# Optimization experiments

Measured on AMD Instinct MI355X. Metric: run time of the kernel, lower is better.

The kernel has to match this reference:

```python
import jax, jax.numpy as jnp
import numpy as np

EPS = 1e-5
N_HEADS = 8
CLAMP = 100.0


def layernorm(x, g, b):
    m = x.mean(-1, keepdims=True)
    v = x.var(-1, keepdims=True)  # biased var, matches torch LayerNorm
    return (x - m) / jnp.sqrt(v + EPS) * g + b


def depthwise7(x, w, b):
    # x: [B,C,H,W], w: [C,1,7,7] depthwise (groups=C), pad=3
    y = jax.lax.conv_general_dilated(
        x, w, window_strides=(1, 1), padding=[(3, 3), (3, 3)],
        dimension_numbers=('NCHW', 'OIHW', 'NCHW'),
        feature_group_count=x.shape[1])
    return y + b[None, :, None, None]


def setup_inputs() -> dict:
    key = jax.random.key(0)
    ks = jax.random.split(key, 12)
    B, N, C = 8, 4096, 512
    KH = 7
    s = 0.02
    return {
        'x': jax.random.normal(ks[0], (B, N, C), jnp.float32),
        'qkv_w': jax.random.normal(ks[1], (C, 3 * C), jnp.float32) * s,
        'qkv_b': jnp.zeros((3 * C,), jnp.float32),
        'out_w': jax.random.normal(ks[2], (C, C), jnp.float32) * s,
        'out_b': jnp.zeros((C,), jnp.float32),
        'pre_g': jnp.ones((C,), jnp.float32),
        'pre_b': jnp.zeros((C,), jnp.float32),
        'lcm_g': jnp.ones((C,), jnp.float32),
        'lcm_b': jnp.zeros((C,), jnp.float32),
        'ci_w': jax.random.normal(ks[3], (C, 1, KH, KH), jnp.float32) * s,
        'ci_b': jnp.zeros((C,), jnp.float32),
        'bn_g': jnp.ones((C,), jnp.float32),
        'bn_b': jnp.zeros((C,), jnp.float32),
        'co_w': jax.random.normal(ks[4], (C, 1, KH, KH), jnp.float32) * s,
        'co_b': jnp.zeros((C,), jnp.float32),
        'H': 64,
        'W': 64,
    }


def reference(x, qkv_w, qkv_b, out_w, out_b, pre_g, pre_b, lcm_g, lcm_b,
              ci_w, ci_b, bn_g, bn_b, co_w, co_b, H, W):
    B, N, C = x.shape
    hd = C // N_HEADS
    normed = layernorm(x, pre_g, pre_b)
    qkv = normed @ qkv_w + qkv_b                       # [B,N,3C]
    qkv = qkv.reshape(B, N, 3, N_HEADS, hd).transpose(2, 0, 3, 1, 4)
    q = jax.nn.relu(qkv[0])                            # [B,h,N,d]
    k = jax.nn.relu(qkv[1])
    v = qkv[2]
    kv = jnp.einsum('bhnd,bhnv->bhdv', k, v)           # O(N d^2) associativity trick
    normalizer = jnp.maximum(k.sum(2, keepdims=True), CLAMP)  # [B,h,1,d]
    attn = jnp.einsum('bhnd,bhdv->bhnv', q, kv)
    denom = jnp.maximum((q * normalizer).sum(-1, keepdims=True), CLAMP)
    attn = attn / denom
    attn = attn.transpose(0, 2, 1, 3).reshape(B, N, C)
    attn = attn @ out_w + out_b
    # Local Concentration Module on lcm_norm(attn)
    t = layernorm(attn, lcm_g, lcm_b)
    xi = t.transpose(0, 2, 1).reshape(B, C, H, W)
    y = depthwise7(xi, ci_w, ci_b)
    y = jax.nn.gelu(y, approximate=False)
    m = y.mean((0, 2, 3), keepdims=True)               # BatchNorm2d training-mode stats
    var = y.var((0, 2, 3), keepdims=True)
    y = (y - m) / jnp.sqrt(var + EPS) * bn_g[None, :, None, None] + bn_b[None, :, None, None]
    y = depthwise7(y, co_w, co_b)
    lcm_out = y.reshape(B, C, N).transpose(0, 2, 1)
    return x + attn + lcm_out
```

## Files before the change

### kernel.cpp

```cpp
#include <hip/hip_runtime.h>
#include <math.h>

typedef short v8s __attribute__((ext_vector_type(8)));
typedef short v4s __attribute__((ext_vector_type(4)));
typedef float v4f __attribute__((ext_vector_type(4)));

__device__ __forceinline__ float b2f(unsigned short u) {
    return __uint_as_float(((unsigned)u) << 16);
}
__device__ __forceinline__ unsigned short f2b(float f) {
    unsigned u = __float_as_uint(f);
    unsigned r = (u + 0x7FFF + ((u >> 16) & 1)) >> 16;
    return (unsigned short)r;
}

__device__ __forceinline__ void gl_lds16(const unsigned short* g, unsigned short* l) {
    __builtin_amdgcn_global_load_lds(
        (const __attribute__((address_space(1))) void*)g,
        (__attribute__((address_space(3))) void*)l,
        16, 0, 0);
}

__global__ __launch_bounds__(256) void zero_fill(float* __restrict__ p, int n) {
    int i = blockIdx.x * 256 + threadIdx.x;
    if (i < n) p[i] = 0.0f;
}

__global__ __launch_bounds__(256) void ln_apply(const float* __restrict__ x,
                                                const float* __restrict__ g,
                                                const float* __restrict__ bt,
                                                unsigned short* __restrict__ out) {
    size_t row = blockIdx.x;
    const float2* p = (const float2*)(x + row * 512);
    int t = threadIdx.x;
    float2 v = p[t];
    float s = v.x + v.y, s2 = v.x * v.x + v.y * v.y;
    for (int o = 32; o > 0; o >>= 1) {
        s += __shfl_down(s, o);
        s2 += __shfl_down(s2, o);
    }
    __shared__ float rs[4], rq[4];
    int wave = t >> 6, lane = t & 63;
    if (lane == 0) { rs[wave] = s; rq[wave] = s2; }
    __syncthreads();
    float ts = rs[0] + rs[1] + rs[2] + rs[3];
    float tq = rq[0] + rq[1] + rq[2] + rq[3];
    float mean = ts * (1.0f / 512.0f);
    float var = tq * (1.0f / 512.0f) - mean * mean;
    float inv = rsqrtf(var + 1e-5f);
    float2 gg = ((const float2*)g)[t];
    float2 bb = ((const float2*)bt)[t];
    ushort2 o2;
    o2.x = f2b((v.x - mean) * inv * gg.x + bb.x);
    o2.y = f2b((v.y - mean) * inv * gg.y + bb.y);
    *(ushort2*)&out[row * 512 + 2 * t] = o2;
}

__global__ __launch_bounds__(256) void transpose_f2b(const float* __restrict__ in,
                                                     unsigned short* __restrict__ out,
                                                     int R, int C) {
    __shared__ unsigned short tile[32][33];
    int c0 = blockIdx.x * 32, r0 = blockIdx.y * 32;
    int tx = threadIdx.x, ty = threadIdx.y;
    for (int j = 0; j < 32; j += 8)
        tile[ty + j][tx] = f2b(in[(size_t)(r0 + ty + j) * C + c0 + tx]);
    __syncthreads();
    for (int j = 0; j < 32; j += 8)
        out[(size_t)(c0 + ty + j) * R + r0 + tx] = tile[tx][ty + j];
}

template <int NB, bool QKV>
__global__ __launch_bounds__(512, 2) void gemm256(const unsigned short* __restrict__ A,
                                                  const unsigned short* __restrict__ Bt,
                                                  const float* __restrict__ bias,
                                                  unsigned short* __restrict__ o0,
                                                  unsigned short* __restrict__ o1,
                                                  unsigned short* __restrict__ o2) {
    __shared__ __align__(16) unsigned short LB[4][2][8192];
    int t = threadIdx.x;
    int wave = t >> 6, lane = t & 63;
    int wm = wave >> 2, wn = wave & 3;
    int mrow = lane & 15, kq4 = lane >> 4;
    int nwg = gridDim.x;
    int cpx = nwg >> 3;
    int bid = blockIdx.x;
    int swz = (bid & 7) * cpx + (bid >> 3);
    int n0 = (swz % NB) * 256;
    int m0 = (swz / NB) * 256;
    const unsigned short* Ab = A + (size_t)m0 * 512;
    const unsigned short* Bb = Bt + (size_t)n0 * 512;
    int g0 = wave * 128 + lane;
    int g1 = g0 + 64;
    int r0 = g0 >> 2, c0 = ((g0 & 3) ^ ((r0 >> 1) & 3)) * 8;
    int r1 = g1 >> 2, c1 = ((g1 & 3) ^ ((r1 >> 1) & 3)) * 8;
    size_t src0 = (size_t)r0 * 512 + c0;
    size_t src1 = (size_t)r1 * 512 + c1;
    unsigned ldsOff0 = wave * 1024;
    unsigned ldsOff1 = wave * 1024 + 512;
    v4f acc[8][4] = {};
    int swr = ((kq4 ^ ((mrow >> 1) & 3)) * 8);

#define STAGE(kt, slot)                                          \
    do {                                                         \
        const unsigned short* aS = Ab + (size_t)(kt) * 32;       \
        const unsigned short* bS = Bb + (size_t)(kt) * 32;       \
        gl_lds16(aS + src0, &LB[slot][0][ldsOff0]);              \
        gl_lds16(aS + src1, &LB[slot][0][ldsOff1]);              \
        gl_lds16(bS + src0, &LB[slot][1][ldsOff0]);              \
        gl_lds16(bS + src1, &LB[slot][1][ldsOff1]);              \
    } while (0)

    STAGE(0, 0);
    STAGE(1, 1);
    for (int kt = 0; kt < 16; ++kt) {
        if (kt < 15) {
            asm volatile("s_waitcnt vmcnt(4)" ::: "memory");
        } else {
            asm volatile("s_waitcnt vmcnt(0)" ::: "memory");
        }
        __builtin_amdgcn_s_barrier();
        asm volatile("" ::: "memory");
        if (kt + 2 < 16) {
            int slot2 = (kt + 2) & 3;
            STAGE(kt + 2, slot2);
        }
        const unsigned short* as = LB[kt & 3][0];
        const unsigned short* bs = LB[kt & 3][1];
        v8s af[8], bf[4];
#pragma unroll
        for (int i = 0; i < 8; i++)
            af[i] = *(const v8s*)&as[(wm * 128 + i * 16 + mrow) * 32 + swr];
#pragma unroll
        for (int j = 0; j < 4; j++)
            bf[j] = *(const v8s*)&bs[(wn * 64 + j * 16 + mrow) * 32 + swr];
        __builtin_amdgcn_s_setprio(1);
#pragma unroll
        for (int i = 0; i < 8; i++)
#pragma unroll
            for (int j = 0; j < 4; j++)
                acc[i][j] = __builtin_amdgcn_mfma_f32_16x16x32_bf16(af[i], bf[j], acc[i][j], 0, 0, 0);
        __builtin_amdgcn_s_setprio(0);
    }
#undef STAGE
    __syncthreads();
    unsigned short* CT = &LB[0][0][0];
    bool doRelu = QKV && (n0 < 1024);
#pragma unroll
    for (int j = 0; j < 4; j++) {
        int col = wn * 64 + j * 16 + mrow;
        float bv = bias[n0 + col];
        int gr = col >> 3;
        int gb = col & 7;
#pragma unroll
        for (int i = 0; i < 8; i++) {
            int rowb = wm * 128 + i * 16 + kq4 * 4;
#pragma unroll
            for (int r = 0; r < 4; r++) {
                int row = rowb + r;
                float v = acc[i][j][r] + bv;
                if (doRelu) v = fmaxf(v, 0.0f);
                CT[row * 256 + ((gr ^ (row & 7)) << 3) + gb] = f2b(v);
            }
        }
    }
    __syncthreads();
    unsigned short* base;
    if (QKV) {
        int seg = n0 >> 9;
        base = (seg == 0) ? o0 : ((seg == 1) ? o1 : o2);
    } else {
        base = o0;
    }
    int cb = n0 & 511;
#pragma unroll
    for (int p = 0; p < 16; p++) {
        int g = p * 512 + t;
        int row = g >> 5, gl = g & 31;
        int phys = gl ^ (row & 7);
        v8s v = *(const v8s*)&CT[row * 256 + (phys << 3)];
        *(v8s*)&base[(size_t)(m0 + row) * 512 + cb + gl * 8] = v;
    }
}

__global__ __launch_bounds__(256) void kv_part(const unsigned short* __restrict__ kbuf,
                                               const unsigned short* __restrict__ vbuf,
                                               float* __restrict__ kvp,
                                               float* __restrict__ ksp) {
    int bh = blockIdx.x;
    int b = bh >> 3, h = bh & 7;
    int nc = blockIdx.y;
    __shared__ __align__(16) unsigned short kb[64 * 64];
    __shared__ __align__(16) unsigned short vb[64 * 64];
    int t = threadIdx.x;
    int dk0 = (t >> 4) * 4;
    int dv0 = (t & 15) * 4;
    float acc[4][4] = {};
    float ks[4] = {};
    int lr = t >> 2, lc = (t & 3) * 16;
    for (int n0 = nc * 128; n0 < nc * 128 + 128; n0 += 64) {
        __syncthreads();
        size_t base = ((size_t)(b * 4096 + n0 + lr)) * 512 + h * 64;
        *(v8s*)&kb[lr * 64 + lc]     = *(const v8s*)&kbuf[base + lc];
        *(v8s*)&kb[lr * 64 + lc + 8] = *(const v8s*)&kbuf[base + lc + 8];
        *(v8s*)&vb[lr * 64 + lc]     = *(const v8s*)&vbuf[base + lc];
        *(v8s*)&vb[lr * 64 + lc + 8] = *(const v8s*)&vbuf[base + lc + 8];
        __syncthreads();
#pragma unroll 4
        for (int nn = 0; nn < 64; nn++) {
            v4s kr = *(const v4s*)&kb[nn * 64 + dk0];
            v4s vr = *(const v4s*)&vb[nn * 64 + dv0];
            float kf[4], vf[4];
#pragma unroll
            for (int i = 0; i < 4; i++) { kf[i] = b2f((unsigned short)kr[i]); vf[i] = b2f((unsigned short)vr[i]); }
#pragma unroll
            for (int i = 0; i < 4; i++) {
#pragma unroll
                for (int j = 0; j < 4; j++) acc[i][j] += kf[i] * vf[j];
            }
            if ((t & 15) == 0) {
#pragma unroll
                for (int i = 0; i < 4; i++) ks[i] += kf[i];
            }
        }
    }
    float* dst = kvp + ((size_t)(bh * 32 + nc)) * 4096;
#pragma unroll
    for (int i = 0; i < 4; i++)
        *(float4*)&dst[(dk0 + i) * 64 + dv0] = make_float4(acc[i][0], acc[i][1], acc[i][2], acc[i][3]);
    if ((t & 15) == 0) {
        float* kd = ksp + ((size_t)(bh * 32 + nc)) * 64;
#pragma unroll
        for (int i = 0; i < 4; i++) kd[dk0 + i] = ks[i];
    }
}

__global__ __launch_bounds__(256) void kv_reduce(const float* __restrict__ kvp,
                                                 const float* __restrict__ ksp,
                                                 float* __restrict__ kvb,
                                                 float* __restrict__ ksum) {
    int tid = blockIdx.x * 256 + threadIdx.x;
    int bh = tid >> 12, e = tid & 4095;
    float s = 0.0f;
#pragma unroll 8
    for (int c = 0; c < 32; c++) s += kvp[((size_t)(bh * 32 + c)) * 4096 + e];
    kvb[(size_t)bh * 4096 + e] = s;
    if (tid < 4096) {
        int bh2 = tid >> 6, dk = tid & 63;
        float t = 0.0f;
#pragma unroll 8
        for (int c = 0; c < 32; c++) t += ksp[((size_t)(bh2 * 32 + c)) * 64 + dk];
        ksum[tid] = t;
    }
}

__global__ __launch_bounds__(256) void attn_kernel(unsigned short* qa,
                                                   const float* __restrict__ kv,
                                                   const float* __restrict__ ksum) {
    int bh = blockIdx.y;
    int b = bh >> 3, h = bh & 7;
    int nt = blockIdx.x;
    __shared__ float kvs[64 * 64];
    __shared__ float nrm[64];
    int t = threadIdx.x;
    for (int i = t; i < 4096; i += 256) kvs[i] = kv[(size_t)bh * 4096 + i];
    if (t < 64) nrm[t] = fmaxf(ksum[bh * 64 + t], 100.0f);
    __syncthreads();
    int n = nt * 256 + t;
    unsigned short* qp = qa + ((size_t)(b * 4096 + n)) * 512 + h * 64;
    float qf[64];
#pragma unroll
    for (int i = 0; i < 64; i += 8) {
        v8s v = *(const v8s*)&qp[i];
#pragma unroll
        for (int j = 0; j < 8; j++) qf[i + j] = b2f((unsigned short)v[j]);
    }
    float denom = 0.0f;
#pragma unroll
    for (int d = 0; d < 64; d++) denom += qf[d] * nrm[d];
    denom = fmaxf(denom, 100.0f);
    float inv = 1.0f / denom;
#pragma unroll
    for (int dv = 0; dv < 64; dv += 16) {
        float o[16] = {};
        for (int dk = 0; dk < 64; dk++) {
            float q = qf[dk];
#pragma unroll
            for (int i = 0; i < 16; i++) o[i] += q * kvs[dk * 64 + dv + i];
        }
#pragma unroll
        for (int i = 0; i < 16; i++) qp[dv + i] = f2b(o[i] * inv);
    }
}

__global__ __launch_bounds__(256) void ln2_transpose(const unsigned short* __restrict__ in,
                                                     const float* __restrict__ g,
                                                     const float* __restrict__ bt,
                                                     unsigned short* __restrict__ out) {
    int bid = blockIdx.x;
    int b = bid >> 6;
    int n0 = (bid & 63) * 64;
    __shared__ float gs[512], bs[512];
    __shared__ __align__(16) unsigned short tile[512 * 64];
    int t = threadIdx.x;
    for (int i = t; i < 512; i += 256) { gs[i] = g[i]; bs[i] = bt[i]; }
    int nl = t >> 2, sub = t & 3;
    const unsigned short* src = in + ((size_t)(b * 4096 + n0 + nl)) * 512 + sub * 8;
    v8s vv[16];
#pragma unroll
    for (int c16 = 0; c16 < 16; c16++)
        vv[c16] = *(const v8s*)&src[c16 * 32];
    float s = 0.f, s2 = 0.f;
#pragma unroll
    for (int c16 = 0; c16 < 16; c16++)
#pragma unroll
        for (int j = 0; j < 8; j++) {
            float f = b2f((unsigned short)vv[c16][j]);
            s += f; s2 += f * f;
        }
    s += __shfl_xor(s, 1); s2 += __shfl_xor(s2, 1);
    s += __shfl_xor(s, 2); s2 += __shfl_xor(s2, 2);
    float mean = s * (1.f / 512.f);
    float var = s2 * (1.f / 512.f) - mean * mean;
    float inv = rsqrtf(var + 1e-5f);
    __syncthreads();
#pragma unroll
    for (int c16 = 0; c16 < 16; c16++) {
        int cb_ = sub * 8 + c16 * 32;
#pragma unroll
        for (int j = 0; j < 8; j++) {
            int c = cb_ + j;
            float f = b2f((unsigned short)vv[c16][j]);
            float y = (f - mean) * inv * gs[c] + bs[c];
            tile[c * 64 + ((((nl >> 3) ^ (c & 7)) << 3) | (nl & 7))] = f2b(y);
        }
    }
    __syncthreads();
    unsigned short* dst = out + ((size_t)b * 512) * 4096 + n0;
#pragma unroll
    for (int p = 0; p < 16; p++) {
        int chunk = p * 256 + t;
        int c = chunk >> 3, gseg = chunk & 7;
        int phys = gseg ^ (c & 7);
        v8s v = *(const v8s*)&tile[c * 64 + phys * 8];
        *(v8s*)&dst[(size_t)c * 4096 + gseg * 8] = v;
    }
}

__global__ __launch_bounds__(256) void dwconv7_gelu(const unsigned short* __restrict__ in,
                                                    const float* __restrict__ w,
                                                    const float* __restrict__ bias,
                                                    unsigned short* __restrict__ out,
                                                    float* __restrict__ bn_sum,
                                                    float* __restrict__ bn_sumsq) {
    int bc = blockIdx.x;
    int c = bc & 511;
    __shared__ float img[70 * 72];
    __shared__ float wsm[49];
    __shared__ float r1[4], r2[4];
    int t = threadIdx.x;
    int tx = t & 63, ty = t >> 6;
    for (int i = t; i < 70 * 72; i += 256) img[i] = 0.0f;
    if (t < 49) wsm[t] = w[c * 49 + t];
    __syncthreads();
    const unsigned short* src = in + (size_t)bc * 4096;
    for (int p = t; p < 4096; p += 256)
        img[((p >> 6) + 3) * 72 + (p & 63) + 3] = b2f(src[p]);
    __syncthreads();
    float wt[49];
#pragma unroll
    for (int i = 0; i < 49; i++) wt[i] = wsm[i];
    float bv = bias[c];
    float acc[16];
#pragma unroll
    for (int i = 0; i < 16; i++) acc[i] = bv;
    int h0 = ty * 16;
#pragma unroll
    for (int rr = 0; rr < 22; rr++) {
        float v[7];
#pragma unroll
        for (int kw = 0; kw < 7; kw++) v[kw] = img[(h0 + rr) * 72 + tx + kw];
#pragma unroll
        for (int kh = 0; kh < 7; kh++) {
            int o = rr - kh;
            if (o >= 0 && o <= 15) {
                float dot = v[0] * wt[kh * 7];
#pragma unroll
                for (int kw = 1; kw < 7; kw++) dot += v[kw] * wt[kh * 7 + kw];
                acc[o] += dot;
            }
        }
    }
    float s = 0.0f, s2 = 0.0f;
    unsigned short* dst = out + (size_t)bc * 4096;
#pragma unroll
    for (int i = 0; i < 16; i++) {
        float a = acc[i];
        float ge = 0.5f * a * (1.0f + erff(a * 0.70710678118f));
        dst[(h0 + i) * 64 + tx] = f2b(ge);
        s += ge;
        s2 += ge * ge;
    }
    for (int o = 32; o > 0; o >>= 1) {
        s += __shfl_down(s, o);
        s2 += __shfl_down(s2, o);
    }
    int lane = t & 63;
    if (lane == 0) { r1[ty] = s; r2[ty] = s2; }
    __syncthreads();
    if (t == 0) {
        atomicAdd(&bn_sum[c], r1[0] + r1[1] + r1[2] + r1[3]);
        atomicAdd(&bn_sumsq[c], r2[0] + r2[1] + r2[2] + r2[3]);
    }
}

__global__ void bn_finalize(const float* __restrict__ s, const float* __restrict__ s2,
                            const float* __restrict__ g, const float* __restrict__ b,
                            float2* __restrict__ ab) {
    int c = blockIdx.x * blockDim.x + threadIdx.x;
    if (c >= 512) return;
    float m = s[c] * (1.0f / 32768.0f);
    float var = s2[c] * (1.0f / 32768.0f) - m * m;
    float inv = rsqrtf(var + 1e-5f);
    float sc = g[c] * inv;
    ab[c] = make_float2(sc, b[c] - m * sc);
}

__global__ __launch_bounds__(256) void dwconv7_bn(const unsigned short* __restrict__ in,
                                                  const float2* __restrict__ bnab,
                                                  const float* __restrict__ w,
                                                  const float* __restrict__ bias,
                                                  unsigned short* __restrict__ out) {
    int bc = blockIdx.x;
    int c = bc & 511;
    __shared__ float img[70 * 72];
    __shared__ float wsm[49];
    int t = threadIdx.x;
    int tx = t & 63, ty = t >> 6;
    for (int i = t; i < 70 * 72; i += 256) img[i] = 0.0f;
    if (t < 49) wsm[t] = w[c * 49 + t];
    __syncthreads();
    float2 ab = bnab[c];
    const unsigned short* src = in + (size_t)bc * 4096;
    for (int p = t; p < 4096; p += 256)
        img[((p >> 6) + 3) * 72 + (p & 63) + 3] = b2f(src[p]) * ab.x + ab.y;
    __syncthreads();
    float wt[49];
#pragma unroll
    for (int i = 0; i < 49; i++) wt[i] = wsm[i];
    float bv = bias[c];
    float acc[16];
#pragma unroll
    for (int i = 0; i < 16; i++) acc[i] = bv;
    int h0 = ty * 16;
#pragma unroll
    for (int rr = 0; rr < 22; rr++) {
        float v[7];
#pragma unroll
        for (int kw = 0; kw < 7; kw++) v[kw] = img[(h0 + rr) * 72 + tx + kw];
#pragma unroll
        for (int kh = 0; kh < 7; kh++) {
            int o = rr - kh;
            if (o >= 0 && o <= 15) {
                float dot = v[0] * wt[kh * 7];
#pragma unroll
                for (int kw = 1; kw < 7; kw++) dot += v[kw] * wt[kh * 7 + kw];
                acc[o] += dot;
            }
        }
    }
    unsigned short* dst = out + (size_t)bc * 4096;
#pragma unroll
    for (int i = 0; i < 16; i++)
        dst[(h0 + i) * 64 + tx] = f2b(acc[i]);
}

__global__ __launch_bounds__(256) void final_add(const float* __restrict__ x,
                                                 const unsigned short* __restrict__ attn,
                                                 const unsigned short* __restrict__ y2,
                                                 float* __restrict__ out) {
    __shared__ unsigned short tile[32][33];
    int b = blockIdx.z;
    int c0 = blockIdx.x * 32, n0 = blockIdx.y * 32;
    int tx = threadIdx.x, ty = threadIdx.y;
    for (int j = 0; j < 32; j += 8)
        tile[ty + j][tx] = y2[((size_t)(b * 512 + c0 + ty + j)) * 4096 + n0 + tx];
    __syncthreads();
    for (int j = 0; j < 32; j += 8) {
        int n = n0 + ty + j, cc = c0 + tx;
        size_t idx = ((size_t)(b * 4096 + n)) * 512 + cc;
        out[idx] = x[idx] + b2f(attn[idx]) + b2f(tile[tx][ty + j]);
    }
}

extern "C" void kernel_launch(void* const* d_in, const int* in_sizes, int n_in,
                              void* d_out, int out_size, void* d_ws, size_t ws_size,
                              hipStream_t stream) {
    const float* x     = (const float*)d_in[0];
    const float* qkv_w = (const float*)d_in[1];
    const float* qkv_b = (const float*)d_in[2];
    const float* out_w = (const float*)d_in[3];
    const float* out_b = (const float*)d_in[4];
    const float* pre_g = (const float*)d_in[5];
    const float* pre_b = (const float*)d_in[6];
    const float* lcm_g = (const float*)d_in[7];
    const float* lcm_b = (const float*)d_in[8];
    const float* ci_w  = (const float*)d_in[9];
    const float* ci_b  = (const float*)d_in[10];
    const float* bn_g  = (const float*)d_in[11];
    const float* bn_b  = (const float*)d_in[12];
    const float* co_w  = (const float*)d_in[13];
    const float* co_b  = (const float*)d_in[14];

    char* ws = (char*)d_ws;
    const size_t SLOT = 33554432;
    unsigned short* S0 = (unsigned short*)(ws);
    unsigned short* S1 = (unsigned short*)(ws + SLOT);
    unsigned short* S2 = (unsigned short*)(ws + 2 * SLOT);
    const size_t MISC = 3 * SLOT;
    unsigned short* wT1 = (unsigned short*)(ws + MISC);
    unsigned short* wT2 = (unsigned short*)(ws + MISC + 1572864);
    float* kvb          = (float*)(ws + MISC + 2097152);
    float* ksum         = (float*)(ws + MISC + 2097152 + 1048576);
    float* bn_sum       = (float*)(ws + MISC + 2097152 + 1048576 + 16384);
    float* bn_sumsq     = (float*)(ws + MISC + 2097152 + 1048576 + 16384 + 2048);
    float2* bnab        = (float2*)(ws + MISC + 3166208);
    float* ksp          = (float*)(ws + MISC + 3170304);
    float* outp         = (float*)d_out;

    unsigned short* normed = (unsigned short*)d_out;
    float* kvp             = (float*)((char*)d_out + SLOT);

    dim3 tb(32, 8);
    transpose_f2b<<<dim3(48, 16), tb, 0, stream>>>(qkv_w, wT1, 512, 1536);
    transpose_f2b<<<dim3(16, 16), tb, 0, stream>>>(out_w, wT2, 512, 512);
    zero_fill<<<4, 256, 0, stream>>>(bn_sum, 1024);
    ln_apply<<<32768, 256, 0, stream>>>(x, pre_g, pre_b, normed);
    gemm256<6, true><<<768, 512, 0, stream>>>(normed, wT1, qkv_b, S0, S1, S2);
    kv_part<<<dim3(64, 32), 256, 0, stream>>>(S1, S2, kvp, ksp);
    kv_reduce<<<1024, 256, 0, stream>>>(kvp, ksp, kvb, ksum);
    attn_kernel<<<dim3(16, 64), 256, 0, stream>>>(S0, kvb, ksum);
    gemm256<2, false><<<256, 512, 0, stream>>>(S0, wT2, out_b, S1, S1, S1);
    ln2_transpose<<<512, 256, 0, stream>>>(S1, lcm_g, lcm_b, S0);
    dwconv7_gelu<<<4096, 256, 0, stream>>>(S0, ci_w, ci_b, S2, bn_sum, bn_sumsq);
    bn_finalize<<<2, 256, 0, stream>>>(bn_sum, bn_sumsq, bn_g, bn_b, bnab);
    dwconv7_bn<<<4096, 256, 0, stream>>>(S2, bnab, co_w, co_b, S0);
    final_add<<<dim3(16, 128, 8), tb, 0, stream>>>(x, S1, S0, outp);
}
```

Before: 515.8 us.

## Shrink GEMM tile to 256x128 with triple buffering, vectorize conv loads and final add

The GEMM tile drops from 256x256 to 256x128 with three LDS stages instead of four, raising the occupancy hint to 4 blocks per CU and doubling the grid. The attention output store, the depthwise-conv image loads and the final residual add switch to 8- and 4-wide vector memory accesses. The final add is flattened to one thread per 4 outputs. The smaller tile lowers data reuse per block and increases B-matrix reloads, traded for more blocks in flight and fewer cycles lost at the tail.

```diff
diff --git a/kernel.cpp b/kernel.cpp
--- a/kernel.cpp
+++ b/kernel.cpp
@@ -70,72 +70,69 @@
 }
 
 template <int NB, bool QKV>
-__global__ __launch_bounds__(512, 2) void gemm256(const unsigned short* __restrict__ A,
+__global__ __launch_bounds__(512, 4) void gemm256(const unsigned short* __restrict__ A,
                                                   const unsigned short* __restrict__ Bt,
                                                   const float* __restrict__ bias,
                                                   unsigned short* __restrict__ o0,
                                                   unsigned short* __restrict__ o1,
                                                   unsigned short* __restrict__ o2) {
-    __shared__ __align__(16) unsigned short LB[4][2][8192];
+    __shared__ __align__(16) unsigned short LB[3][12288];
     int t = threadIdx.x;
     int wave = t >> 6, lane = t & 63;
-    int wm = wave >> 2, wn = wave & 3;
+    int wm = wave >> 1, wn = wave & 1;
     int mrow = lane & 15, kq4 = lane >> 4;
     int nwg = gridDim.x;
     int cpx = nwg >> 3;
     int bid = blockIdx.x;
     int swz = (bid & 7) * cpx + (bid >> 3);
-    int n0 = (swz % NB) * 256;
+    int n0 = (swz % NB) * 128;
     int m0 = (swz / NB) * 256;
     const unsigned short* Ab = A + (size_t)m0 * 512;
     const unsigned short* Bb = Bt + (size_t)n0 * 512;
-    int g0 = wave * 128 + lane;
-    int g1 = g0 + 64;
-    int r0 = g0 >> 2, c0 = ((g0 & 3) ^ ((r0 >> 1) & 3)) * 8;
-    int r1 = g1 >> 2, c1 = ((g1 & 3) ^ ((r1 >> 1) & 3)) * 8;
-    size_t src0 = (size_t)r0 * 512 + c0;
-    size_t src1 = (size_t)r1 * 512 + c1;
-    unsigned ldsOff0 = wave * 1024;
-    unsigned ldsOff1 = wave * 1024 + 512;
-    v4f acc[8][4] = {};
+    int rA0 = t >> 2;
+    int cA0 = (((t & 3) ^ ((rA0 >> 1) & 3)) * 8);
+    int rA1 = 128 + (t >> 2);
+    int cA1 = (((t & 3) ^ ((rA1 >> 1) & 3)) * 8);
+    size_t srcA0 = (size_t)rA0 * 512 + cA0;
+    size_t srcA1 = (size_t)rA1 * 512 + cA1;
+    unsigned offA0 = wave * 512;
+    unsigned offA1 = 4096 + wave * 512;
+    unsigned offB  = 8192 + wave * 512;
+    v4f acc[4][4] = {};
     int swr = ((kq4 ^ ((mrow >> 1) & 3)) * 8);
 
 #define STAGE(kt, slot)                                          \
     do {                                                         \
         const unsigned short* aS = Ab + (size_t)(kt) * 32;       \
         const unsigned short* bS = Bb + (size_t)(kt) * 32;       \
-        gl_lds16(aS + src0, &LB[slot][0][ldsOff0]);              \
-        gl_lds16(aS + src1, &LB[slot][0][ldsOff1]);              \
-        gl_lds16(bS + src0, &LB[slot][1][ldsOff0]);              \
-        gl_lds16(bS + src1, &LB[slot][1][ldsOff1]);              \
+        gl_lds16(aS + srcA0, &LB[slot][offA0]);                  \
+        gl_lds16(aS + srcA1, &LB[slot][offA1]);                  \
+        gl_lds16(bS + srcA0, &LB[slot][offB]);                   \
     } while (0)
 
     STAGE(0, 0);
     STAGE(1, 1);
     for (int kt = 0; kt < 16; ++kt) {
         if (kt < 15) {
-            asm volatile("s_waitcnt vmcnt(4)" ::: "memory");
+            asm volatile("s_waitcnt vmcnt(3)" ::: "memory");
         } else {
             asm volatile("s_waitcnt vmcnt(0)" ::: "memory");
         }
         __builtin_amdgcn_s_barrier();
         asm volatile("" ::: "memory");
-        if (kt + 2 < 16) {
-            int slot2 = (kt + 2) & 3;
-            STAGE(kt + 2, slot2);
-        }
-        const unsigned short* as = LB[kt & 3][0];
-        const unsigned short* bs = LB[kt & 3][1];
-        v8s af[8], bf[4];
-#pragma unroll
-        for (int i = 0; i < 8; i++)
-            af[i] = *(const v8s*)&as[(wm * 128 + i * 16 + mrow) * 32 + swr];
+        if (kt + 2 < 16) STAGE(kt + 2, (kt + 2) % 3);
+        const unsigned short* as = LB[kt % 3];
+        const unsigned short* bs = LB[kt % 3] + 8192;
+        v8s af[4], bf[4];
+#pragma unroll
+        for (int i = 0; i < 4; i++)
+            af[i] = *(const v8s*)&as[(wm * 64 + i * 16 + mrow) * 32 + swr];
 #pragma unroll
         for (int j = 0; j < 4; j++)
             bf[j] = *(const v8s*)&bs[(wn * 64 + j * 16 + mrow) * 32 + swr];
         __builtin_amdgcn_s_setprio(1);
 #pragma unroll
-        for (int i = 0; i < 8; i++)
+        for (int i = 0; i < 4; i++)
 #pragma unroll
             for (int j = 0; j < 4; j++)
                 acc[i][j] = __builtin_amdgcn_mfma_f32_16x16x32_bf16(af[i], bf[j], acc[i][j], 0, 0, 0);
@@ -143,7 +140,7 @@
     }
 #undef STAGE
     __syncthreads();
-    unsigned short* CT = &LB[0][0][0];
+    unsigned short* CT = &LB[0][0];
     bool doRelu = QKV && (n0 < 1024);
 #pragma unroll
     for (int j = 0; j < 4; j++) {
@@ -152,32 +149,34 @@
         int gr = col >> 3;
         int gb = col & 7;
 #pragma unroll
-        for (int i = 0; i < 8; i++) {
-            int rowb = wm * 128 + i * 16 + kq4 * 4;
+        for (int i = 0; i < 4; i++) {
+            int rowb = wm * 64 + i * 16 + kq4 * 4;
 #pragma unroll
             for (int r = 0; r < 4; r++) {
                 int row = rowb + r;
                 float v = acc[i][j][r] + bv;
                 if (doRelu) v = fmaxf(v, 0.0f);
-                CT[row * 256 + ((gr ^ (row & 7)) << 3) + gb] = f2b(v);
+                CT[row * 128 + ((gr ^ (row & 7)) << 3) + gb] = f2b(v);
             }
         }
     }
     __syncthreads();
     unsigned short* base;
+    int cb;
     if (QKV) {
         int seg = n0 >> 9;
         base = (seg == 0) ? o0 : ((seg == 1) ? o1 : o2);
+        cb = n0 & 511;
     } else {
         base = o0;
-    }
-    int cb = n0 & 511;
-#pragma unroll
-    for (int p = 0; p < 16; p++) {
+        cb = n0;
+    }
+#pragma unroll
+    for (int p = 0; p < 8; p++) {
         int g = p * 512 + t;
-        int row = g >> 5, gl = g & 31;
+        int row = g >> 4, gl = g & 15;
         int phys = gl ^ (row & 7);
-        v8s v = *(const v8s*)&CT[row * 256 + (phys << 3)];
+        v8s v = *(const v8s*)&CT[row * 128 + (phys << 3)];
         *(v8s*)&base[(size_t)(m0 + row) * 512 + cb + gl * 8] = v;
     }
 }
@@ -287,8 +286,14 @@
 #pragma unroll
             for (int i = 0; i < 16; i++) o[i] += q * kvs[dk * 64 + dv + i];
         }
-#pragma unroll
-        for (int i = 0; i < 16; i++) qp[dv + i] = f2b(o[i] * inv);
+        v8s ov0, ov1;
+#pragma unroll
+        for (int i = 0; i < 8; i++) {
+            ov0[i] = (short)f2b(o[i] * inv);
+            ov1[i] = (short)f2b(o[i + 8] * inv);
+        }
+        *(v8s*)&qp[dv] = ov0;
+        *(v8s*)&qp[dv + 8] = ov1;
     }
 }
 
@@ -363,8 +368,13 @@
     if (t < 49) wsm[t] = w[c * 49 + t];
     __syncthreads();
     const unsigned short* src = in + (size_t)bc * 4096;
-    for (int p = t; p < 4096; p += 256)
-        img[((p >> 6) + 3) * 72 + (p & 63) + 3] = b2f(src[p]);
+#pragma unroll
+    for (int q = t; q < 512; q += 256) {
+        v8s v = *(const v8s*)&src[q * 8];
+        float* ip = &img[((q >> 3) + 3) * 72 + (q & 7) * 8 + 3];
+#pragma unroll
+        for (int j = 0; j < 8; j++) ip[j] = b2f((unsigned short)v[j]);
+    }
     __syncthreads();
     float wt[49];
 #pragma unroll
@@ -441,8 +451,13 @@
     __syncthreads();
     float2 ab = bnab[c];
     const unsigned short* src = in + (size_t)bc * 4096;
-    for (int p = t; p < 4096; p += 256)
-        img[((p >> 6) + 3) * 72 + (p & 63) + 3] = b2f(src[p]) * ab.x + ab.y;
+#pragma unroll
+    for (int q = t; q < 512; q += 256) {
+        v8s v = *(const v8s*)&src[q * 8];
+        float* ip = &img[((q >> 3) + 3) * 72 + (q & 7) * 8 + 3];
+#pragma unroll
+        for (int j = 0; j < 8; j++) ip[j] = b2f((unsigned short)v[j]) * ab.x + ab.y;
+    }
     __syncthreads();
     float wt[49];
 #pragma unroll
@@ -478,18 +493,26 @@
                                                  const unsigned short* __restrict__ attn,
                                                  const unsigned short* __restrict__ y2,
                                                  float* __restrict__ out) {
-    __shared__ unsigned short tile[32][33];
+    __shared__ unsigned short tile[32][36];
     int b = blockIdx.z;
     int c0 = blockIdx.x * 32, n0 = blockIdx.y * 32;
-    int tx = threadIdx.x, ty = threadIdx.y;
-    for (int j = 0; j < 32; j += 8)
-        tile[ty + j][tx] = y2[((size_t)(b * 512 + c0 + ty + j)) * 4096 + n0 + tx];
-    __syncthreads();
-    for (int j = 0; j < 32; j += 8) {
-        int n = n0 + ty + j, cc = c0 + tx;
-        size_t idx = ((size_t)(b * 4096 + n)) * 512 + cc;
-        out[idx] = x[idx] + b2f(attn[idx]) + b2f(tile[tx][ty + j]);
-    }
+    int t = threadIdx.x;
+    {
+        int c = t >> 3, n4 = (t & 7) * 4;
+        ushort4 v = *(const ushort4*)&y2[((size_t)(b * 512 + c0 + c)) * 4096 + n0 + n4];
+        tile[c][n4] = v.x; tile[c][n4 + 1] = v.y; tile[c][n4 + 2] = v.z; tile[c][n4 + 3] = v.w;
+    }
+    __syncthreads();
+    int nl = t >> 3, cl = (t & 7) * 4;
+    size_t idx = ((size_t)(b * 4096 + n0 + nl)) * 512 + c0 + cl;
+    float4 xv = *(const float4*)&x[idx];
+    ushort4 av = *(const ushort4*)&attn[idx];
+    float4 o;
+    o.x = xv.x + b2f(av.x) + b2f(tile[cl][nl]);
+    o.y = xv.y + b2f(av.y) + b2f(tile[cl + 1][nl]);
+    o.z = xv.z + b2f(av.z) + b2f(tile[cl + 2][nl]);
+    o.w = xv.w + b2f(av.w) + b2f(tile[cl + 3][nl]);
+    *(float4*)&out[idx] = o;
 }
 
 extern "C" void kernel_launch(void* const* d_in, const int* in_sizes, int n_in,
@@ -535,14 +558,14 @@
     transpose_f2b<<<dim3(16, 16), tb, 0, stream>>>(out_w, wT2, 512, 512);
     zero_fill<<<4, 256, 0, stream>>>(bn_sum, 1024);
     ln_apply<<<32768, 256, 0, stream>>>(x, pre_g, pre_b, normed);
-    gemm256<6, true><<<768, 512, 0, stream>>>(normed, wT1, qkv_b, S0, S1, S2);
+    gemm256<12, true><<<1536, 512, 0, stream>>>(normed, wT1, qkv_b, S0, S1, S2);
     kv_part<<<dim3(64, 32), 256, 0, stream>>>(S1, S2, kvp, ksp);
     kv_reduce<<<1024, 256, 0, stream>>>(kvp, ksp, kvb, ksum);
     attn_kernel<<<dim3(16, 64), 256, 0, stream>>>(S0, kvb, ksum);
-    gemm256<2, false><<<256, 512, 0, stream>>>(S0, wT2, out_b, S1, S1, S1);
+    gemm256<4, false><<<512, 512, 0, stream>>>(S0, wT2, out_b, S1, S1, S1);
     ln2_transpose<<<512, 256, 0, stream>>>(S1, lcm_g, lcm_b, S0);
     dwconv7_gelu<<<4096, 256, 0, stream>>>(S0, ci_w, ci_b, S2, bn_sum, bn_sumsq);
     bn_finalize<<<2, 256, 0, stream>>>(bn_sum, bn_sumsq, bn_g, bn_b, bnab);
     dwconv7_bn<<<4096, 256, 0, stream>>>(S2, bnab, co_w, co_b, S0);
-    final_add<<<dim3(16, 128, 8), tb, 0, stream>>>(x, S1, S0, outp);
-}
+    final_add<<<dim3(16, 128, 8), tb.x * tb.y, 0, stream>>>(x, S1, S0, outp);
+}
```

New measurement: 518.9 us. About the same (+0.6%).
